# Kernel optimization log

Hardware: AMD Instinct MI355X
Metric: run time of the kernel (lower is better)

Reference implementation:

```python
import jax, jax.numpy as jnp
import numpy as np

B, N, DIM = 2, 2048, 1024
H, DH = 16, 64            # num query heads, head dim (single shared kv head)
CTX_N, CTX_DIM = 256, 1024

def setup_inputs() -> dict:
    key = jax.random.key(0)
    ks = jax.random.split(key, 8)
    s = lambda fan: 1.0 / np.sqrt(fan)
    return {
        'x': jax.random.normal(ks[0], (B, N, DIM), jnp.float32),
        'context': jax.random.normal(ks[1], (B, CTX_N, CTX_DIM), jnp.float32),
        'g1': jnp.ones((DIM,), jnp.float32),
        'Wq': jax.random.normal(ks[2], (DIM, H * DH), jnp.float32) * s(DIM),
        'Wkv': jax.random.normal(ks[3], (DIM, 2 * DH), jnp.float32) * s(DIM),
        'null_kv': jax.random.normal(ks[4], (2, DH), jnp.float32) * s(DH),
        'ctx_g': jnp.ones((CTX_DIM,), jnp.float32),
        'ctx_b': jnp.zeros((CTX_DIM,), jnp.float32),
        'Wc': jax.random.normal(ks[5], (CTX_DIM, 2 * DH), jnp.float32) * s(CTX_DIM),
        'bc': jnp.zeros((2 * DH,), jnp.float32),
        'Wout': jax.random.normal(ks[6], (H * DH, DIM), jnp.float32) * s(H * DH),
        'g2': jnp.ones((DIM,), jnp.float32),
    }

def _ln_g(t, g, eps):
    # custom LayerNorm: scale only, no bias, population variance
    m = jnp.mean(t, axis=-1, keepdims=True)
    v = jnp.var(t, axis=-1, keepdims=True)
    return (t - m) / jnp.sqrt(v + eps) * g

def reference(x, context, g1, Wq, Wkv, null_kv, ctx_g, ctx_b, Wc, bc, Wout, g2):
    b, n, _ = x.shape
    scale = DH ** -0.5
    h = _ln_g(x, g1, 1e-5)                              # [b,n,dim]
    q = (h @ Wq).reshape(b, n, H, DH).transpose(0, 2, 1, 3) * scale  # [b,H,n,d]
    k, v = jnp.split(h @ Wkv, 2, axis=-1)               # each [b,n,d] (single kv head)
    # null kv token
    nk = jnp.broadcast_to(null_kv[0], (b, 1, DH))
    nv = jnp.broadcast_to(null_kv[1], (b, 1, DH))
    k = jnp.concatenate((k, nk), axis=-2)
    v = jnp.concatenate((v, nv), axis=-2)
    # context kv tokens (standard flax LayerNorm: scale+bias, eps=1e-6)
    cm = jnp.mean(context, axis=-1, keepdims=True)
    cv_ = jnp.var(context, axis=-1, keepdims=True)
    ch = (context - cm) / jnp.sqrt(cv_ + 1e-6) * ctx_g + ctx_b
    ck, cvv = jnp.split(ch @ Wc + bc, 2, axis=-1)       # [b,ctx_n,d]
    k = jnp.concatenate((k, ck), axis=-2)               # [b,j,d]
    v = jnp.concatenate((v, cvv), axis=-2)
    sim = jnp.einsum('bhid,bjd->bhij', q, k)            # shared kv head broadcast
    attn = jax.nn.softmax(sim, axis=-1)
    out = jnp.einsum('bhij,bjd->bhid', attn, v)
    out = out.transpose(0, 2, 1, 3).reshape(b, n, H * DH)
    out = out @ Wout
    return _ln_g(out, g2, 1e-5)
```

## Files before the change

### kernel.cpp

```cpp
#include <hip/hip_runtime.h>

typedef __attribute__((ext_vector_type(4)))  float  f32x4;
typedef __attribute__((ext_vector_type(16))) float  f32x16;
typedef __attribute__((ext_vector_type(8)))  short  s16x8;

#define DEVI __device__ __forceinline__

constexpr int Bb   = 2;
constexpr int Nn   = 2048;
constexpr int Hh   = 16;
constexpr int DHc  = 64;
constexpr int CTXN = 256;
constexpr int Jv   = Nn + 1 + CTXN;
constexpr int JP   = 2432;
constexpr int NPAD = JP - Jv;
constexpr int QKVN = Hh*DHc + 2*DHc;

DEVI unsigned short f2bf(float f) {
    union { float f; unsigned u; } v; v.f = f;
    unsigned r = v.u + 0x7fffu + ((v.u >> 16) & 1u);
    return (unsigned short)(r >> 16);
}
DEVI float bf2f(unsigned short h) {
    union { unsigned u; float f; } v; v.u = ((unsigned)h) << 16;
    return v.f;
}
DEVI unsigned cvt_pk_bf(float lo, float hi) {
    unsigned r;
    asm("v_cvt_pk_bf16_f32 %0, %1, %2" : "=v"(r) : "v"(lo), "v"(hi));
    return r;
}
DEVI float exp2v(float x) {
    float r;
    asm("v_exp_f32 %0, %1" : "=v"(r) : "v"(x));
    return r;
}
DEVI void gl_lds16(const void* g, void* l) {
    __builtin_amdgcn_global_load_lds(
        (__attribute__((address_space(1))) void*)g,
        (__attribute__((address_space(3))) void*)l,
        16, 0, 0);
}

__global__ __launch_bounds__(256) void k_pre(const float* __restrict__ Wq,
                                             const float* __restrict__ Wkv,
                                             const float* __restrict__ Wc,
                                             const float* __restrict__ Wout,
                                             const float* __restrict__ x,
                                             const float* __restrict__ ctx,
                                             const float* __restrict__ g1,
                                             const float* __restrict__ cg,
                                             const float* __restrict__ cb,
                                             unsigned short* __restrict__ WqkvT,
                                             unsigned short* __restrict__ WcT,
                                             unsigned short* __restrict__ WoutT,
                                             unsigned short* __restrict__ h,
                                             unsigned short* __restrict__ ch,
                                             float qscale) {
    int bxg = blockIdx.x;
    if (bxg < 2304) {
        __shared__ float tile[32][33];
        int bx = bxg % 72, by = bxg / 72;
        const float* in; unsigned short* out; int C; float scale; int cb_;
        if (bx < 32)      { in = Wq;   out = WqkvT;               C = 1024; scale = qscale; cb_ = bx; }
        else if (bx < 36) { in = Wkv;  out = WqkvT + 1024 * 1024; C = 128;  scale = 1.0f;  cb_ = bx - 32; }
        else if (bx < 40) { in = Wc;   out = WcT;                 C = 128;  scale = 1.0f;  cb_ = bx - 36; }
        else              { in = Wout; out = WoutT;               C = 1024; scale = 1.0f;  cb_ = bx - 40; }
        int tx = threadIdx.x & 31, ty = threadIdx.x >> 5;
        int r0 = by * 32, c0 = cb_ * 32;
#pragma unroll
        for (int i = 0; i < 32; i += 8)
            tile[ty + i][tx] = in[(size_t)(r0 + ty + i) * C + c0 + tx];
        __syncthreads();
#pragma unroll
        for (int i = 0; i < 32; i += 8)
            out[(size_t)(c0 + ty + i) * 1024 + r0 + tx] = f2bf(tile[tx][ty + i] * scale);
    } else {
        int row = bxg - 2304, tid = threadIdx.x;
        bool isx = row < 4096;
        const float* rp = isx ? x + (size_t)row * 1024 : ctx + (size_t)(row - 4096) * 1024;
        const float* g  = isx ? g1 : cg;
        float eps = isx ? 1e-5f : 1e-6f;
        unsigned short* o = isx ? h + (size_t)row * 1024 : ch + (size_t)(row - 4096) * 1024;

        f32x4 v = *(const f32x4*)(rp + tid * 4);
        float s = v.x + v.y + v.z + v.w;
        float q = v.x * v.x + v.y * v.y + v.z * v.z + v.w * v.w;
#pragma unroll
        for (int m = 32; m; m >>= 1) { s += __shfl_down(s, m, 64); q += __shfl_down(q, m, 64); }
        __shared__ float ss[4], sq[4];
        int wid = tid >> 6, lane = tid & 63;
        if (lane == 0) { ss[wid] = s; sq[wid] = q; }
        __syncthreads();
        s = ss[0] + ss[1] + ss[2] + ss[3];
        q = sq[0] + sq[1] + sq[2] + sq[3];
        float mean = s * (1.0f / 1024.0f);
        float var  = q * (1.0f / 1024.0f) - mean * mean;
        float rstd = rsqrtf(var + eps);
        f32x4 gg = *(const f32x4*)(g + tid * 4);
        f32x4 r;
#pragma unroll
        for (int e = 0; e < 4; e++) r[e] = (v[e] - mean) * rstd * gg[e];
        if (!isx) {
            f32x4 bb = *(const f32x4*)(cb + tid * 4);
#pragma unroll
            for (int e = 0; e < 4; e++) r[e] += bb[e];
        }
        uint2 ov = make_uint2(cvt_pk_bf(r[0], r[1]), cvt_pk_bf(r[2], r[3]));
        *(uint2*)(o + tid * 4) = ov;
    }
}

__global__ __launch_bounds__(256) void k_ln_out(const unsigned short* __restrict__ in,
                                                const float* __restrict__ g,
                                                float* __restrict__ out) {
    int row = blockIdx.x, tid = threadIdx.x;
    const unsigned short* rp = in + (size_t)row * 1024;
    uint2 raw = *(const uint2*)(rp + tid * 4);
    f32x4 v;
    v.x = bf2f((unsigned short)(raw.x & 0xffff));
    v.y = bf2f((unsigned short)(raw.x >> 16));
    v.z = bf2f((unsigned short)(raw.y & 0xffff));
    v.w = bf2f((unsigned short)(raw.y >> 16));
    float s = v.x + v.y + v.z + v.w;
    float q = v.x * v.x + v.y * v.y + v.z * v.z + v.w * v.w;
#pragma unroll
    for (int m = 32; m; m >>= 1) { s += __shfl_down(s, m, 64); q += __shfl_down(q, m, 64); }
    __shared__ float ss[4], sq[4];
    int wid = tid >> 6, lane = tid & 63;
    if (lane == 0) { ss[wid] = s; sq[wid] = q; }
    __syncthreads();
    s = ss[0] + ss[1] + ss[2] + ss[3];
    q = sq[0] + sq[1] + sq[2] + sq[3];
    float mean = s * (1.0f / 1024.0f);
    float var  = q * (1.0f / 1024.0f) - mean * mean;
    float rstd = rsqrtf(var + 1e-5f);
    f32x4 gg = *(const f32x4*)(g + tid * 4);
    f32x4 r;
#pragma unroll
    for (int e = 0; e < 4; e++) r[e] = (v[e] - mean) * rstd * gg[e];
    *(f32x4*)(out + (size_t)row * 1024 + tid * 4) = r;
}

template<int OUT_BF16>
DEVI void gemm128(unsigned short* Al, unsigned short* Bl,
                  const unsigned short* __restrict__ A,
                  const unsigned short* __restrict__ BT,
                  void* __restrict__ C,
                  int M, int N, int K, int bn, int bm) {
    int tid = threadIdx.x;
    int wid = tid >> 6, lane = tid & 63;
    int wm = wid >> 1, wn = wid & 1;
    int lr = lane & 15, lg = lane >> 4;
    int r8 = lane >> 3;
    int sl = (lane & 7) ^ r8;

    const unsigned short* Ag = A  + (size_t)(bm * 128 + wid * 32 + r8) * K + sl * 8;
    const unsigned short* Bg = BT + (size_t)(bn * 128 + wid * 32 + r8) * K + sl * 8;

    f32x4 acc[4][4] = {};
    int nk = K >> 6;
#pragma unroll 1
    for (int s = 0; s < nk; ++s) {
        int k0 = s << 6;
        __syncthreads();
#pragma unroll
        for (int i = 0; i < 4; i++) {
            gl_lds16(Ag + (size_t)i * 8 * K + k0, Al + wid * 2048 + i * 512);
            gl_lds16(Bg + (size_t)i * 8 * K + k0, Bl + wid * 2048 + i * 512);
        }
        __syncthreads();
#pragma unroll
        for (int kk = 0; kk < 2; kk++) {
            int co = ((kk * 4 + lg) ^ (lr & 7)) * 8;
            s16x8 af[4], bf[4];
#pragma unroll
            for (int mi = 0; mi < 4; mi++)
                af[mi] = *(const s16x8*)&Al[(wm * 64 + mi * 16 + lr) * 64 + co];
#pragma unroll
            for (int ni = 0; ni < 4; ni++)
                bf[ni] = *(const s16x8*)&Bl[(wn * 64 + ni * 16 + lr) * 64 + co];
#pragma unroll
            for (int mi = 0; mi < 4; mi++)
#pragma unroll
                for (int ni = 0; ni < 4; ni++)
                    acc[mi][ni] = __builtin_amdgcn_mfma_f32_16x16x32_bf16(af[mi], bf[ni], acc[mi][ni], 0, 0, 0);
        }
    }
#pragma unroll
    for (int mi = 0; mi < 4; mi++)
#pragma unroll
        for (int r = 0; r < 4; r++) {
            int row = bm * 128 + wm * 64 + mi * 16 + lg * 4 + r;
#pragma unroll
            for (int ni = 0; ni < 4; ni++) {
                int col = bn * 128 + wn * 64 + ni * 16 + lr;
                float val = acc[mi][ni][r];
                if (OUT_BF16)
                    ((unsigned short*)C)[(size_t)row * N + col] = f2bf(val);
                else
                    ((float*)C)[(size_t)row * N + col] = val;
            }
        }
}

__global__ __launch_bounds__(256) void k_gemm_qkv(const unsigned short* __restrict__ h,
                                                  const unsigned short* __restrict__ WqkvT,
                                                  unsigned short* __restrict__ qkv,
                                                  const unsigned short* __restrict__ ch,
                                                  const unsigned short* __restrict__ WcT,
                                                  unsigned short* __restrict__ ckv) {
    __shared__ unsigned short SA[128 * 64];
    __shared__ unsigned short SB[128 * 64];
    int g = blockIdx.x;
    if (g < 288) {
        int id = (g & 7) * 36 + (g >> 3);
        gemm128<1>(SA, SB, h, WqkvT, qkv, 4096, 1152, 1024, id % 9, id / 9);
    } else {
        gemm128<1>(SA, SB, ch, WcT, ckv, 512, 128, 1024, 0, g - 288);
    }
}

__global__ __launch_bounds__(256) void k_gemm_out(const unsigned short* __restrict__ aout,
                                                  const unsigned short* __restrict__ WoutT,
                                                  unsigned short* __restrict__ preout) {
    __shared__ unsigned short SA[128 * 64];
    __shared__ unsigned short SB[128 * 64];
    int g = blockIdx.x;
    int id = (g & 7) * 32 + (g >> 3);
    gemm128<1>(SA, SB, aout, WoutT, preout, 4096, 1024, 1024, id % 8, id / 8);
}

__global__ __launch_bounds__(256) void k_assemble_kv(const unsigned short* __restrict__ qkv,
                                                     const unsigned short* __restrict__ ckv,
                                                     const float* __restrict__ nkv,
                                                     const float* __restrict__ bc,
                                                     unsigned short* __restrict__ Kb,
                                                     unsigned short* __restrict__ Vt) {
    __shared__ unsigned short Vl[64][66];
    int bid = blockIdx.x;
    int b = bid / 38, jt = bid % 38;
    int j0 = jt * 64;
    int tid = threadIdx.x;
    int jl = tid >> 2, qu = tid & 3;
    int j = j0 + jl;

    unsigned short kbuf[16], vbuf[16];
    if (j < Nn) {
        const unsigned short* r = qkv + (size_t)(b * Nn + j) * QKVN + Hh * DHc;
        *(s16x8*)&kbuf[0] = *(const s16x8*)(r + qu * 16);
        *(s16x8*)&kbuf[8] = *(const s16x8*)(r + qu * 16 + 8);
        *(s16x8*)&vbuf[0] = *(const s16x8*)(r + 64 + qu * 16);
        *(s16x8*)&vbuf[8] = *(const s16x8*)(r + 64 + qu * 16 + 8);
    } else if (j == Nn) {
#pragma unroll
        for (int i = 0; i < 16; i++) {
            kbuf[i] = f2bf(nkv[qu * 16 + i]);
            vbuf[i] = f2bf(nkv[64 + qu * 16 + i]);
        }
    } else if (j < Jv) {
        const unsigned short* r = ckv + (size_t)(b * CTXN + (j - Nn - 1)) * 128;
#pragma unroll
        for (int i = 0; i < 16; i++) {
            kbuf[i] = f2bf(bf2f(r[qu * 16 + i]) + bc[qu * 16 + i]);
            vbuf[i] = f2bf(bf2f(r[64 + qu * 16 + i]) + bc[64 + qu * 16 + i]);
        }
    } else {
#pragma unroll
        for (int i = 0; i < 16; i++) { kbuf[i] = 0; vbuf[i] = 0; }
    }
    *(s16x8*)(Kb + ((size_t)b * JP + j) * 64 + qu * 16)     = *(s16x8*)&kbuf[0];
    *(s16x8*)(Kb + ((size_t)b * JP + j) * 64 + qu * 16 + 8) = *(s16x8*)&kbuf[8];
#pragma unroll
    for (int i = 0; i < 16; i++) Vl[jl][qu * 16 + i] = vbuf[i];
    __syncthreads();
#pragma unroll
    for (int it = 0; it < 2; it++) {
        int d = it * 32 + (tid >> 3), pt = tid & 7;
        unsigned short ob[8];
#pragma unroll
        for (int i = 0; i < 8; i++) ob[i] = Vl[pt * 8 + i][d];
        *(s16x8*)(Vt + ((size_t)b * 64 + d) * JP + j0 + pt * 8) = *(s16x8*)&ob[0];
    }
}

__global__ __launch_bounds__(512) void k_attn(const unsigned short* __restrict__ qkv,
                                              const unsigned short* __restrict__ Kb,
                                              const unsigned short* __restrict__ Vt,
                                              unsigned short* __restrict__ aout) {
    __shared__ unsigned short KV[2][2][2][64 * 64];

    int bid = blockIdx.x;
    int qt = bid & 15, h = (bid >> 4) & 15, b = bid >> 8;
    int tid = threadIdx.x, wid = tid >> 6, lane = tid & 63;
    int tm = wid >> 2, tw = wid & 3;
    int l31 = lane & 31, hi = lane >> 5;
    int n0 = qt * 128 + tw * 32;
    int r8 = lane >> 3;
    int sl = (lane & 7) ^ r8;
    int x7 = l31 & 7;
    int jb = tm * 1216;

    s16x8 qf[4];
#pragma unroll
    for (int kk = 0; kk < 4; kk++)
        qf[kk] = *(const s16x8*)(qkv + (size_t)(b * Nn + n0 + l31) * QKVN + h * 64 + kk * 16 + hi * 8);

    f32x16 O0 = {}, O1 = {};
    float Lv = 0.0f;

    const unsigned short* Kg = Kb + ((size_t)b * JP + jb + tw * 16 + r8) * 64 + sl * 8;
    const unsigned short* Vg = Vt + ((size_t)b * 64 + tw * 16 + r8) * JP + jb + sl * 8;

    auto stage = [&](int t, int buf) {
#pragma unroll
        for (int i = 0; i < 2; i++) {
            gl_lds16(Kg + ((size_t)t * 64 + i * 8) * 64, &KV[tm][buf][0][tw * 1024 + i * 512]);
            gl_lds16(Vg + (size_t)i * 8 * JP + t * 64,   &KV[tm][buf][1][tw * 1024 + i * 512]);
        }
    };

    auto build_pf = [&](const f32x16& s, int w) -> s16x8 {
        unsigned c0 = cvt_pk_bf(s[8 * w + 0], s[8 * w + 1]);
        unsigned c1 = cvt_pk_bf(s[8 * w + 2], s[8 * w + 3]);
        unsigned c2 = cvt_pk_bf(s[8 * w + 4], s[8 * w + 5]);
        unsigned c3 = cvt_pk_bf(s[8 * w + 6], s[8 * w + 7]);
        asm("v_permlane32_swap_b32 %0, %1" : "+v"(c0), "+v"(c2));
        asm("v_permlane32_swap_b32 %0, %1" : "+v"(c1), "+v"(c3));
        union { unsigned u[4]; s16x8 v; } pu;
        pu.u[0] = c0; pu.u[1] = c1; pu.u[2] = c2; pu.u[3] = c3;
        return pu.v;
    };

    stage(0, 0);
    asm volatile("s_waitcnt vmcnt(0)" ::: "memory");
    asm volatile("s_barrier" ::: "memory");
    int cur = 0;
#pragma unroll 1
    for (int t = 0; t < 19; ++t) {
        if (t < 18) {
            stage(t + 1, cur ^ 1);
            asm volatile("s_waitcnt vmcnt(4)" ::: "memory");
        } else {
            asm volatile("s_waitcnt vmcnt(0)" ::: "memory");
        }
        asm volatile("s_barrier" ::: "memory");
        __builtin_amdgcn_sched_barrier(0);
        const unsigned short* Kl = &KV[tm][cur][0][0];
        const unsigned short* Vl = &KV[tm][cur][1][0];

        f32x16 s0 = {}, s1 = {};
        __builtin_amdgcn_s_setprio(1);
#pragma unroll
        for (int kk = 0; kk < 4; kk++) {
            int co = ((kk * 2 + hi) ^ x7) * 8;
            s16x8 k0 = *(const s16x8*)&Kl[l31 * 64 + co];
            s16x8 k1 = *(const s16x8*)&Kl[(32 + l31) * 64 + co];
            s0 = __builtin_amdgcn_mfma_f32_32x32x16_bf16(k0, qf[kk], s0, 0, 0, 0);
            s1 = __builtin_amdgcn_mfma_f32_32x32x16_bf16(k1, qf[kk], s1, 0, 0, 0);
        }
        __builtin_amdgcn_s_setprio(0);

        float sum = 0.0f;
#pragma unroll
        for (int r = 0; r < 16; r++) { s0[r] = exp2v(s0[r]); sum += s0[r]; }
#pragma unroll
        for (int r = 0; r < 16; r++) { s1[r] = exp2v(s1[r]); sum += s1[r]; }
        Lv += sum;

        __builtin_amdgcn_s_setprio(1);
#pragma unroll
        for (int ks = 0; ks < 4; ks++) {
            s16x8 pf = (ks < 2) ? build_pf(s0, ks & 1) : build_pf(s1, ks & 1);
            int co = ((ks * 2 + hi) ^ x7) * 8;
            s16x8 v0 = *(const s16x8*)&Vl[l31 * 64 + co];
            s16x8 v1 = *(const s16x8*)&Vl[(32 + l31) * 64 + co];
            O0 = __builtin_amdgcn_mfma_f32_32x32x16_bf16(v0, pf, O0, 0, 0, 0);
            O1 = __builtin_amdgcn_mfma_f32_32x32x16_bf16(v1, pf, O1, 0, 0, 0);
        }
        __builtin_amdgcn_s_setprio(0);
        __builtin_amdgcn_sched_barrier(0);
        asm volatile("s_barrier" ::: "memory");
        cur ^= 1;
    }

    Lv += __shfl_xor(Lv, 32, 64);
    if (tm == 1) Lv -= (float)NPAD;

    float* Ob = (float*)&KV[0][0][0][0];
    float* Ml = Ob + 4 * 64 * 33;
    unsigned short* slabs = (unsigned short*)(Ml + 4 * 64);

    __syncthreads();
    if (tm == 1) {
        float* dst = Ob + ((size_t)tw * 64 + lane) * 33;
#pragma unroll
        for (int r = 0; r < 16; r++) { dst[r] = O0[r]; dst[16 + r] = O1[r]; }
        Ml[tw * 64 + lane] = Lv;
    }
    __syncthreads();
    if (tm == 0) {
        const float* src = Ob + ((size_t)tw * 64 + lane) * 33;
        float rl = 1.0f / (Lv + Ml[tw * 64 + lane]);

        unsigned short* slab = slabs + tw * 2304;
#pragma unroll
        for (int rq = 0; rq < 4; rq++) {
            uint2 w0 = make_uint2(
                cvt_pk_bf((O0[rq * 4 + 0] + src[rq * 4 + 0]) * rl,
                          (O0[rq * 4 + 1] + src[rq * 4 + 1]) * rl),
                cvt_pk_bf((O0[rq * 4 + 2] + src[rq * 4 + 2]) * rl,
                          (O0[rq * 4 + 3] + src[rq * 4 + 3]) * rl));
            *(uint2*)&slab[l31 * 72 + rq * 8 + hi * 4] = w0;
            uint2 w1 = make_uint2(
                cvt_pk_bf((O1[rq * 4 + 0] + src[16 + rq * 4 + 0]) * rl,
                          (O1[rq * 4 + 1] + src[16 + rq * 4 + 1]) * rl),
                cvt_pk_bf((O1[rq * 4 + 2] + src[16 + rq * 4 + 2]) * rl,
                          (O1[rq * 4 + 3] + src[16 + rq * 4 + 3]) * rl));
            *(uint2*)&slab[l31 * 72 + 32 + rq * 8 + hi * 4] = w1;
        }
        int q = lane >> 1, half = lane & 1;
        const s16x8* srcq = (const s16x8*)&slab[q * 72 + half * 32];
        s16x8 o0 = srcq[0], o1 = srcq[1], o2 = srcq[2], o3 = srcq[3];
        unsigned short* gdst = aout + (size_t)(b * Nn + n0 + q) * 1024 + h * 64 + half * 32;
        *(s16x8*)gdst = o0;
        *((s16x8*)gdst + 1) = o1;
        *((s16x8*)gdst + 2) = o2;
        *((s16x8*)gdst + 3) = o3;
    }
}

extern "C" void kernel_launch(void* const* d_in, const int* in_sizes, int n_in,
                              void* d_out, int out_size, void* d_ws, size_t ws_size,
                              hipStream_t stream) {
    const float* x    = (const float*)d_in[0];
    const float* ctx  = (const float*)d_in[1];
    const float* g1   = (const float*)d_in[2];
    const float* Wq   = (const float*)d_in[3];
    const float* Wkv  = (const float*)d_in[4];
    const float* nkv  = (const float*)d_in[5];
    const float* ctxg = (const float*)d_in[6];
    const float* ctxb = (const float*)d_in[7];
    const float* Wc   = (const float*)d_in[8];
    const float* bc   = (const float*)d_in[9];
    const float* Wout = (const float*)d_in[10];
    const float* g2   = (const float*)d_in[11];
    float* out = (float*)d_out;

    char* w = (char*)d_ws;
    unsigned short* h_    = (unsigned short*)w; w += (size_t)4096 * 1024 * 2;
    unsigned short* ch    = (unsigned short*)w; w += (size_t)512 * 1024 * 2;
    unsigned short* WqkvT = (unsigned short*)w; w += (size_t)1152 * 1024 * 2;
    unsigned short* WcT   = (unsigned short*)w; w += (size_t)128 * 1024 * 2;
    unsigned short* WoutT = (unsigned short*)w; w += (size_t)1024 * 1024 * 2;
    unsigned short* qkv   = (unsigned short*)w; w += (size_t)4096 * QKVN * 2;
    unsigned short* ckv   = (unsigned short*)w; w += (size_t)512 * 128 * 2;
    unsigned short* Kb    = (unsigned short*)w; w += (size_t)Bb * JP * 64 * 2;
    unsigned short* Vt    = (unsigned short*)w; w += (size_t)Bb * 64 * JP * 2;
    unsigned short* aout  = (unsigned short*)w; w += (size_t)4096 * 1024 * 2;

    const float qscale = 0.125f * 1.4426950408889634f;

    k_pre<<<6912, 256, 0, stream>>>(Wq, Wkv, Wc, Wout, x, ctx, g1, ctxg, ctxb,
                                    WqkvT, WcT, WoutT, h_, ch, qscale);

    k_gemm_qkv<<<292, 256, 0, stream>>>(h_, WqkvT, qkv, ch, WcT, ckv);

    k_assemble_kv<<<Bb * 38, 256, 0, stream>>>(qkv, ckv, nkv, bc, Kb, Vt);

    k_attn<<<Bb * Hh * (Nn / 128), 512, 0, stream>>>(qkv, Kb, Vt, aout);

    k_gemm_out<<<256, 256, 0, stream>>>(aout, WoutT, h_);
    k_ln_out<<<4096, 256, 0, stream>>>(h_, g2, out);
}
```

Measured before the change: 109.8 us.

## Double-buffer LDS tiles in GEMM to overlap global loads with MFMA

Converts the shared 128x128 GEMM helper from single-buffered to double-buffered LDS staging. The next K-slice's global-to-LDS loads are issued before computing the current slice, with explicit vmcnt waits and raw barriers. This is meant to hide global memory latency behind MFMA work in the QKV and output projection GEMMs. It doubles LDS use per block to 64 KB, which may lower occupancy.

Measured after the change: 105.3 us. -4.0%, faster.

```diff
diff --git a/kernel.cpp b/kernel.cpp
--- a/kernel.cpp
+++ b/kernel.cpp
@@ -143,7 +143,7 @@
 }
 
 template<int OUT_BF16>
-DEVI void gemm128(unsigned short* Al, unsigned short* Bl,
+DEVI void gemm128(unsigned short* SAb, unsigned short* SBb,
                   const unsigned short* __restrict__ A,
                   const unsigned short* __restrict__ BT,
                   void* __restrict__ C,
@@ -158,18 +158,33 @@
     const unsigned short* Ag = A  + (size_t)(bm * 128 + wid * 32 + r8) * K + sl * 8;
     const unsigned short* Bg = BT + (size_t)(bn * 128 + wid * 32 + r8) * K + sl * 8;
 
+    auto stage = [&](int buf, int s) {
+        int k0 = s << 6;
+        unsigned short* SA = SAb + buf * (128 * 64);
+        unsigned short* SB = SBb + buf * (128 * 64);
+#pragma unroll
+        for (int i = 0; i < 4; i++) {
+            gl_lds16(Ag + (size_t)i * 8 * K + k0, SA + wid * 2048 + i * 512);
+            gl_lds16(Bg + (size_t)i * 8 * K + k0, SB + wid * 2048 + i * 512);
+        }
+    };
+
     f32x4 acc[4][4] = {};
     int nk = K >> 6;
+    stage(0, 0);
+    int cur = 0;
 #pragma unroll 1
     for (int s = 0; s < nk; ++s) {
-        int k0 = s << 6;
-        __syncthreads();
-#pragma unroll
-        for (int i = 0; i < 4; i++) {
-            gl_lds16(Ag + (size_t)i * 8 * K + k0, Al + wid * 2048 + i * 512);
-            gl_lds16(Bg + (size_t)i * 8 * K + k0, Bl + wid * 2048 + i * 512);
-        }
-        __syncthreads();
+        if (s + 1 < nk) {
+            stage(cur ^ 1, s + 1);
+            asm volatile("s_waitcnt vmcnt(8)" ::: "memory");
+        } else {
+            asm volatile("s_waitcnt vmcnt(0)" ::: "memory");
+        }
+        __builtin_amdgcn_s_barrier();
+        __builtin_amdgcn_sched_barrier(0);
+        const unsigned short* Al = SAb + cur * (128 * 64);
+        const unsigned short* Bl = SBb + cur * (128 * 64);
 #pragma unroll
         for (int kk = 0; kk < 2; kk++) {
             int co = ((kk * 4 + lg) ^ (lr & 7)) * 8;
@@ -186,6 +201,9 @@
                 for (int ni = 0; ni < 4; ni++)
                     acc[mi][ni] = __builtin_amdgcn_mfma_f32_16x16x32_bf16(af[mi], bf[ni], acc[mi][ni], 0, 0, 0);
         }
+        __builtin_amdgcn_sched_barrier(0);
+        __builtin_amdgcn_s_barrier();
+        cur ^= 1;
     }
 #pragma unroll
     for (int mi = 0; mi < 4; mi++)
@@ -210,25 +228,25 @@
                                                   const unsigned short* __restrict__ ch,
                                                   const unsigned short* __restrict__ WcT,
                                                   unsigned short* __restrict__ ckv) {
-    __shared__ unsigned short SA[128 * 64];
-    __shared__ unsigned short SB[128 * 64];
+    __shared__ unsigned short SA[2][128 * 64];
+    __shared__ unsigned short SB[2][128 * 64];
     int g = blockIdx.x;
     if (g < 288) {
         int id = (g & 7) * 36 + (g >> 3);
-        gemm128<1>(SA, SB, h, WqkvT, qkv, 4096, 1152, 1024, id % 9, id / 9);
+        gemm128<1>(&SA[0][0], &SB[0][0], h, WqkvT, qkv, 4096, 1152, 1024, id % 9, id / 9);
     } else {
-        gemm128<1>(SA, SB, ch, WcT, ckv, 512, 128, 1024, 0, g - 288);
+        gemm128<1>(&SA[0][0], &SB[0][0], ch, WcT, ckv, 512, 128, 1024, 0, g - 288);
     }
 }
 
 __global__ __launch_bounds__(256) void k_gemm_out(const unsigned short* __restrict__ aout,
                                                   const unsigned short* __restrict__ WoutT,
                                                   unsigned short* __restrict__ preout) {
-    __shared__ unsigned short SA[128 * 64];
-    __shared__ unsigned short SB[128 * 64];
+    __shared__ unsigned short SA[2][128 * 64];
+    __shared__ unsigned short SB[2][128 * 64];
     int g = blockIdx.x;
     int id = (g & 7) * 32 + (g >> 3);
-    gemm128<1>(SA, SB, aout, WoutT, preout, 4096, 1024, 1024, id % 8, id / 8);
+    gemm128<1>(&SA[0][0], &SB[0][0], aout, WoutT, preout, 4096, 1024, 1024, id % 8, id / 8);
 }
 
 __global__ __launch_bounds__(256) void k_assemble_kv(const unsigned short* __restrict__ qkv,
```
